# Kernel optimization log

Measured on AMD Instinct MI355X. Metric: run time of the kernel, lower is better.

## Reference

```python
import jax, jax.numpy as jnp
import numpy as np

N_NODES = 50000
N_EDGES = 600000
IN_CH = 128
HID = 128   # 2 * out_channels
OUT = 64


def setup_inputs() -> dict:
    key = jax.random.key(0)
    ks = jax.random.split(key, 8)
    x = jax.random.normal(ks[0], (N_NODES, IN_CH), dtype=jnp.float32)
    edge_index = jax.random.randint(ks[1], (2, N_EDGES), 0, N_NODES, dtype=jnp.int64)
    edge_weight = jax.random.uniform(ks[2], (N_EDGES,), dtype=jnp.float32)
    # GCNConv params: glorot-style linear weight (no lin bias), plus conv bias
    W1 = jax.random.normal(ks[3], (IN_CH, HID), dtype=jnp.float32) / np.sqrt(IN_CH)
    b1 = jnp.zeros((HID,), dtype=jnp.float32)
    W2 = jax.random.normal(ks[4], (HID, OUT), dtype=jnp.float32) / np.sqrt(HID)
    b2 = jnp.zeros((OUT,), dtype=jnp.float32)
    return {"x": x, "edge_index": edge_index, "edge_weight": edge_weight,
            "W1": W1, "b1": b1, "W2": W2, "b2": b2}


def reference(x, edge_index, edge_weight, W1, b1, W2, b2):
    n = x.shape[0]
    row, col = edge_index[0], edge_index[1]
    # gcn_norm with add_self_loops=True (self-loop weight = 1.0):
    # deg[j] = sum_{(i,j) in E} w_ij + 1
    deg = jax.ops.segment_sum(edge_weight, col, num_segments=n) + 1.0
    dis = jnp.where(deg > 0, jax.lax.rsqrt(deg), 0.0)  # deg^{-1/2}
    norm = dis[row] * edge_weight * dis[col]           # [E]
    self_norm = dis * dis                              # [N], self-loop weight 1

    def gcn(h, W, b):
        hW = h @ W                                      # [N, F_out]
        # gather source features, scale by norm, scatter-add to destinations
        agg = jax.ops.segment_sum(norm[:, None] * hW[row], col, num_segments=n)
        return agg + self_norm[:, None] * hW + b

    h = jax.nn.elu(gcn(x, W1, b1))
    alpha = jax.nn.softplus(gcn(h, W2, b2)) + 1e-4
    return alpha
```

## Files before the change

### kernel.cpp

```cpp
#include <hip/hip_runtime.h>
#include <math.h>

typedef unsigned int uint32;
typedef __attribute__((ext_vector_type(8))) short bf16x8;
typedef __attribute__((ext_vector_type(4))) float f32x4;

#define CAP 64

__device__ inline unsigned short f2bf(float f) {
    unsigned int u = __float_as_uint(f);
    return (unsigned short)((u + 0x7fffu + ((u >> 16) & 1u)) >> 16);
}
__device__ inline float bf2f(unsigned short u) {
    return __uint_as_float((unsigned int)u << 16);
}
__device__ inline float softplus_f(float x) {
    return fmaxf(x, 0.f) + log1pf(expf(-fabsf(x)));
}


template<int NC, bool BF16IN>
__device__ void mfma_gemm_body(const void* Xv, const float* __restrict__ W,
                               unsigned short* __restrict__ tabY, int M, int bid) {
    constexpr int PAD = 40;
    __shared__ unsigned short As[128 * PAD];
    __shared__ unsigned short Bs[NC * PAD];

    const int t = threadIdx.x;
    const int lane = t & 63;
    const int wv = t >> 6;
    const int row0 = bid * 128;
    const int l15 = lane & 15, l4 = lane >> 4;

    const int wrow = (NC == 128) ? (wv >> 1) * 64 : wv * 32;
    const int wcol = (NC == 128) ? (wv & 1) * 64 : 0;
    constexpr int NI = (NC == 128) ? 4 : 2;
    constexpr int NJ = 4;

    f32x4 acc[NI][NJ];
#pragma unroll
    for (int i = 0; i < NI; ++i)
#pragma unroll
        for (int j = 0; j < NJ; ++j) acc[i][j] = (f32x4)(0.f);

    for (int k0 = 0; k0 < 128; k0 += 32) {
        __syncthreads();
        if (BF16IN) {
            const unsigned short* X = (const unsigned short*)Xv;
#pragma unroll
            for (int q = 0; q < 2; ++q) {
                int chunk = t * 2 + q;
                int r = chunk >> 2, k8 = chunk & 3;
                int gr = row0 + r;
                uint4 v = make_uint4(0, 0, 0, 0);
                if (gr < M) v = *(const uint4*)&X[(size_t)gr * 128 + k0 + k8 * 8];
                *(uint4*)&As[r * PAD + k8 * 8] = v;
            }
        } else {
            const float* X = (const float*)Xv;
#pragma unroll
            for (int q = 0; q < 4; ++q) {
                int chunk = t * 4 + q;
                int r = chunk >> 3, k4 = chunk & 7;
                int gr = row0 + r;
                float4 v = make_float4(0.f, 0.f, 0.f, 0.f);
                if (gr < M) v = *(const float4*)&X[(size_t)gr * 128 + k0 + k4 * 4];
                ushort4 o;
                o.x = f2bf(v.x); o.y = f2bf(v.y); o.z = f2bf(v.z); o.w = f2bf(v.w);
                *(ushort4*)&As[r * PAD + k4 * 4] = o;
            }
        }
        if (NC == 128) {
#pragma unroll
            for (int q = 0; q < 4; ++q) {
                int chunk = t * 4 + q;
                int kr = chunk >> 5, c4 = chunk & 31;
                float4 v = *(const float4*)&W[(size_t)(k0 + kr) * NC + c4 * 4];
                Bs[(c4 * 4 + 0) * PAD + kr] = f2bf(v.x);
                Bs[(c4 * 4 + 1) * PAD + kr] = f2bf(v.y);
                Bs[(c4 * 4 + 2) * PAD + kr] = f2bf(v.z);
                Bs[(c4 * 4 + 3) * PAD + kr] = f2bf(v.w);
            }
        } else {
#pragma unroll
            for (int q = 0; q < 2; ++q) {
                int chunk = t * 2 + q;
                int kr = chunk >> 4, c4 = chunk & 15;
                float4 v = *(const float4*)&W[(size_t)(k0 + kr) * NC + c4 * 4];
                Bs[(c4 * 4 + 0) * PAD + kr] = f2bf(v.x);
                Bs[(c4 * 4 + 1) * PAD + kr] = f2bf(v.y);
                Bs[(c4 * 4 + 2) * PAD + kr] = f2bf(v.z);
                Bs[(c4 * 4 + 3) * PAD + kr] = f2bf(v.w);
            }
        }
        __syncthreads();

        bf16x8 af[NI], bfr[NJ];
#pragma unroll
        for (int i = 0; i < NI; ++i)
            af[i] = *(const bf16x8*)&As[(wrow + i * 16 + l15) * PAD + l4 * 8];
#pragma unroll
        for (int j = 0; j < NJ; ++j)
            bfr[j] = *(const bf16x8*)&Bs[(wcol + j * 16 + l15) * PAD + l4 * 8];
#pragma unroll
        for (int i = 0; i < NI; ++i)
#pragma unroll
            for (int j = 0; j < NJ; ++j)
                acc[i][j] = __builtin_amdgcn_mfma_f32_16x16x32_bf16(
                    af[i], bfr[j], acc[i][j], 0, 0, 0);
    }

#pragma unroll
    for (int i = 0; i < NI; ++i)
#pragma unroll
        for (int r = 0; r < 4; ++r) {
            int grow = row0 + wrow + i * 16 + l4 * 4 + r;
            if (grow < M) {
#pragma unroll
                for (int j = 0; j < NJ; ++j)
                    tabY[(size_t)grow * NC + wcol + j * 16 + l15] = f2bf(acc[i][j][r]);
            }
        }
}


__global__ __launch_bounds__(256) void k_fused1(const float* __restrict__ X,
                                                const float* __restrict__ W,
                                                unsigned short* __restrict__ tabY, int M,
                                                const int* __restrict__ row,
                                                const int* __restrict__ col,
                                                const float* __restrict__ ew,
                                                int* __restrict__ cnt,
                                                uint32* __restrict__ csr,
                                                int E, int Ggemm) {
    if ((int)blockIdx.x < Ggemm) {
        mfma_gemm_body<128, false>(X, W, tabY, M, blockIdx.x);
    } else {
        int e = (blockIdx.x - Ggemm) * 256 + threadIdx.x;
        if (e < E) {
            int c = col[e];
            int pos = atomicAdd(&cnt[c], 1);
            if (pos < CAP)
                csr[(size_t)c * CAP + pos] = ((uint32)f2bf(ew[e]) << 16) | (uint32)row[e];
        }
    }
}

__global__ __launch_bounds__(256) void k_gemm64(const unsigned short* __restrict__ H,
                                                const float* __restrict__ W,
                                                unsigned short* __restrict__ tabY, int M) {
    mfma_gemm_body<64, true>(H, W, tabY, M, blockIdx.x);
}

__global__ void k_deg_dis(uint32* __restrict__ csr, const int* __restrict__ cnt,
                          float* __restrict__ dis, int n) {
    int i = blockIdx.x * 256 + threadIdx.x;
    if (i >= n) return;
    int deg = min(cnt[i], CAP);
    size_t beg = (size_t)i * CAP;
    float s = 1.0f;
    for (int p = 0; p < deg; ++p) s += bf2f(csr[beg + p] >> 16);
    dis[i] = rsqrtf(s);
    int pe = (deg + 3) & ~3;
    for (int p = deg; p < pe; ++p) csr[beg + p] = 0;
}


__global__ __launch_bounds__(256) void k_agg128(const unsigned short* __restrict__ tab,
                                                const uint32* __restrict__ csr,
                                                const int* __restrict__ cnt,
                                                const float* __restrict__ dis,
                                                const float* __restrict__ b,
                                                unsigned short* __restrict__ hout, int N) {
    int node = blockIdx.x * 4 + (threadIdx.x >> 6);
    if (node >= N) return;
    int lane = threadIdx.x & 63;
    int li = lane & 31, grp = lane >> 5;
    int deg = min(cnt[node], CAP);
    size_t beg = (size_t)node * CAP;

    float a0 = 0.f, a1 = 0.f, a2 = 0.f, a3 = 0.f;

    for (int p = 0; p < deg; p += 4) {
        uint4 c4 = *(const uint4*)&csr[beg + p];
        uint32 ea = grp ? c4.y : c4.x;
        uint32 eb = grp ? c4.w : c4.z;
        int sa = ea & 0xffffu;
        int sb = eb & 0xffffu;
        float wa = bf2f((unsigned short)(ea >> 16)) * dis[sa];
        float wb = bf2f((unsigned short)(eb >> 16)) * dis[sb];
        ushort4 ta = *(const ushort4*)&tab[(size_t)sa * 128 + li * 4];
        ushort4 tb = *(const ushort4*)&tab[(size_t)sb * 128 + li * 4];
        a0 = fmaf(wa, bf2f(ta.x), a0); a1 = fmaf(wa, bf2f(ta.y), a1);
        a2 = fmaf(wa, bf2f(ta.z), a2); a3 = fmaf(wa, bf2f(ta.w), a3);
        a0 = fmaf(wb, bf2f(tb.x), a0); a1 = fmaf(wb, bf2f(tb.y), a1);
        a2 = fmaf(wb, bf2f(tb.z), a2); a3 = fmaf(wb, bf2f(tb.w), a3);
    }
    a0 += __shfl_xor(a0, 32);
    a1 += __shfl_xor(a1, 32);
    a2 += __shfl_xor(a2, 32);
    a3 += __shfl_xor(a3, 32);

    if (grp == 0) {
        float d = dis[node], sn = d * d;
        ushort4 hv = *(const ushort4*)&tab[(size_t)node * 128 + li * 4];
        float4 bb = *(const float4*)&b[li * 4];
        float v0 = d * a0 + sn * bf2f(hv.x) + bb.x;
        float v1 = d * a1 + sn * bf2f(hv.y) + bb.y;
        float v2 = d * a2 + sn * bf2f(hv.z) + bb.z;
        float v3 = d * a3 + sn * bf2f(hv.w) + bb.w;
        v0 = v0 > 0.f ? v0 : expm1f(v0);
        v1 = v1 > 0.f ? v1 : expm1f(v1);
        v2 = v2 > 0.f ? v2 : expm1f(v2);
        v3 = v3 > 0.f ? v3 : expm1f(v3);
        ushort4 o;
        o.x = f2bf(v0); o.y = f2bf(v1); o.z = f2bf(v2); o.w = f2bf(v3);
        *(ushort4*)&hout[(size_t)node * 128 + li * 4] = o;
    }
}

__global__ __launch_bounds__(256) void k_agg64(const unsigned short* __restrict__ tab,
                                               const uint32* __restrict__ csr,
                                               const int* __restrict__ cnt,
                                               const float* __restrict__ dis,
                                               const float* __restrict__ b,
                                               float* __restrict__ out, int N) {
    int node = blockIdx.x * 4 + (threadIdx.x >> 6);
    if (node >= N) return;
    int lane = threadIdx.x & 63;
    int li = lane & 31, grp = lane >> 5;
    int deg = min(cnt[node], CAP);
    size_t beg = (size_t)node * CAP;

    float a0 = 0.f, a1 = 0.f;

    for (int p = 0; p < deg; p += 4) {
        uint4 c4 = *(const uint4*)&csr[beg + p];
        uint32 ea = grp ? c4.y : c4.x;
        uint32 eb = grp ? c4.w : c4.z;
        int sa = ea & 0xffffu;
        int sb = eb & 0xffffu;
        float wa = bf2f((unsigned short)(ea >> 16)) * dis[sa];
        float wb = bf2f((unsigned short)(eb >> 16)) * dis[sb];
        ushort2 ta = *(const ushort2*)&tab[(size_t)sa * 64 + li * 2];
        ushort2 tb = *(const ushort2*)&tab[(size_t)sb * 64 + li * 2];
        a0 = fmaf(wa, bf2f(ta.x), a0); a1 = fmaf(wa, bf2f(ta.y), a1);
        a0 = fmaf(wb, bf2f(tb.x), a0); a1 = fmaf(wb, bf2f(tb.y), a1);
    }
    a0 += __shfl_xor(a0, 32);
    a1 += __shfl_xor(a1, 32);

    if (grp == 0) {
        float d = dis[node], sn = d * d;
        ushort2 hv = *(const ushort2*)&tab[(size_t)node * 64 + li * 2];
        float2 bb = *(const float2*)&b[li * 2];
        float v0 = d * a0 + sn * bf2f(hv.x) + bb.x;
        float v1 = d * a1 + sn * bf2f(hv.y) + bb.y;
        v0 = softplus_f(v0) + 1e-4f;
        v1 = softplus_f(v1) + 1e-4f;
        *(float2*)&out[(size_t)node * 64 + li * 2] = make_float2(v0, v1);
    }
}


extern "C" void kernel_launch(void* const* d_in, const int* in_sizes, int n_in,
                              void* d_out, int out_size, void* d_ws, size_t ws_size,
                              hipStream_t stream) {
    const float* x  = (const float*)d_in[0];
    const int*   ei = (const int*)d_in[1];
    const float* ew = (const float*)d_in[2];
    const float* W1 = (const float*)d_in[3];
    const float* b1 = (const float*)d_in[4];
    const float* W2 = (const float*)d_in[5];
    const float* b2 = (const float*)d_in[6];

    const int N = in_sizes[0] / 128;
    const int E = in_sizes[2];
    const int* row = ei;
    const int* col = ei + E;

    const int Na = (N + 63) & ~63;

    char* base = (char*)d_ws;
    float*  dis  = (float*)base;                    base += (size_t)Na * 4;
    int*    cnt  = (int*)base;                      base += (size_t)Na * 4;
    uint32* csr  = (uint32*)base;                   base += (size_t)Na * CAP * 4;
    unsigned short* tab1 = (unsigned short*)base;   base += (size_t)N * 128 * 2;
    unsigned short* h    = (unsigned short*)base;   base += (size_t)N * 128 * 2;
    unsigned short* tab2 = (unsigned short*)base;   base += (size_t)N * 64 * 2;

    const int gN = (N + 255) / 256;
    const int gE = (E + 255) / 256;
    const int Ggemm = (N + 127) / 128;

    hipMemsetAsync(cnt, 0, (size_t)N * 4, stream);

    k_fused1<<<Ggemm + gE, 256, 0, stream>>>(x, W1, tab1, N, row, col, ew,
                                             cnt, csr, E, Ggemm);

    k_deg_dis<<<gN, 256, 0, stream>>>(csr, cnt, dis, N);

    k_agg128<<<(N + 3) / 4, 256, 0, stream>>>(tab1, csr, cnt, dis, b1, h, N);

    k_gemm64<<<Ggemm, 256, 0, stream>>>(h, W2, tab2, N);
    k_agg64<<<(N + 3) / 4, 256, 0, stream>>>(tab2, csr, cnt, dis, b2,
                                             (float*)d_out, N);
}
```

Before: 126.8 us.

## Prescale features by deg^-1/2 to drop per-edge dis gathers in aggregation

Factors the symmetric normalization so source rows are prescaled by dis (a new warp-per-node kernel for layer 1, the GEMM epilogue for layer 2). The aggregation loops then no longer gather dis[src] per edge. The degree computation becomes a wave-wide shuffle reduction, the epilogues use both half-waves with fast exp/log intrinsics, and the loop runs to the padded degree. The cost is an extra read-modify-write of tab1 and slightly different bf16 rounding and transcendental accuracy.

```diff
diff --git a/kernel.cpp b/kernel.cpp
--- a/kernel.cpp
+++ b/kernel.cpp
@@ -14,13 +14,17 @@
 __device__ inline float bf2f(unsigned short u) {
     return __uint_as_float((unsigned int)u << 16);
 }
-__device__ inline float softplus_f(float x) {
-    return fmaxf(x, 0.f) + log1pf(expf(-fabsf(x)));
-}
-
-
-template<int NC, bool BF16IN>
+__device__ inline float softplus_fast(float x) {
+    return fmaxf(x, 0.f) + __logf(1.f + __expf(-fabsf(x)));
+}
+__device__ inline float elu_fast(float v) {
+    return v > 0.f ? v : (__expf(v) - 1.f);
+}
+
+
+template<int NC, bool BF16IN, bool SCALE>
 __device__ void mfma_gemm_body(const void* Xv, const float* __restrict__ W,
+                               const float* __restrict__ dscale,
                                unsigned short* __restrict__ tabY, int M, int bid) {
     constexpr int PAD = 40;
     __shared__ unsigned short As[128 * PAD];
@@ -116,9 +120,11 @@
         for (int r = 0; r < 4; ++r) {
             int grow = row0 + wrow + i * 16 + l4 * 4 + r;
             if (grow < M) {
+                float dd = SCALE ? dscale[grow] : 1.0f;
 #pragma unroll
                 for (int j = 0; j < NJ; ++j)
-                    tabY[(size_t)grow * NC + wcol + j * 16 + l15] = f2bf(acc[i][j][r]);
+                    tabY[(size_t)grow * NC + wcol + j * 16 + l15] =
+                        f2bf(dd * acc[i][j][r]);
             }
         }
 }
@@ -134,7 +140,7 @@
                                                 uint32* __restrict__ csr,
                                                 int E, int Ggemm) {
     if ((int)blockIdx.x < Ggemm) {
-        mfma_gemm_body<128, false>(X, W, tabY, M, blockIdx.x);
+        mfma_gemm_body<128, false, false>(X, W, nullptr, tabY, M, blockIdx.x);
     } else {
         int e = (blockIdx.x - Ggemm) * 256 + threadIdx.x;
         if (e < E) {
@@ -148,21 +154,35 @@
 
 __global__ __launch_bounds__(256) void k_gemm64(const unsigned short* __restrict__ H,
                                                 const float* __restrict__ W,
+                                                const float* __restrict__ dis,
                                                 unsigned short* __restrict__ tabY, int M) {
-    mfma_gemm_body<64, true>(H, W, tabY, M, blockIdx.x);
-}
-
-__global__ void k_deg_dis(uint32* __restrict__ csr, const int* __restrict__ cnt,
-                          float* __restrict__ dis, int n) {
-    int i = blockIdx.x * 256 + threadIdx.x;
-    if (i >= n) return;
-    int deg = min(cnt[i], CAP);
-    size_t beg = (size_t)i * CAP;
-    float s = 1.0f;
-    for (int p = 0; p < deg; ++p) s += bf2f(csr[beg + p] >> 16);
-    dis[i] = rsqrtf(s);
-    int pe = (deg + 3) & ~3;
-    for (int p = deg; p < pe; ++p) csr[beg + p] = 0;
+    mfma_gemm_body<64, true, true>(H, W, dis, tabY, M, blockIdx.x);
+}
+
+
+__global__ __launch_bounds__(256) void k_disscale(uint32* __restrict__ csr,
+                                                  const int* __restrict__ cnt,
+                                                  float* __restrict__ dis,
+                                                  unsigned short* __restrict__ tab1,
+                                                  int N) {
+    int node = blockIdx.x * 4 + (threadIdx.x >> 6);
+    if (node >= N) return;
+    int lane = threadIdx.x & 63;
+    int deg = min(cnt[node], CAP);
+    int degp = (deg + 3) & ~3;
+    size_t beg = (size_t)node * CAP;
+
+    float w = (lane < deg) ? bf2f((unsigned short)(csr[beg + lane] >> 16)) : 0.f;
+    if (lane >= deg && lane < degp) csr[beg + lane] = 0;
+#pragma unroll
+    for (int m = 1; m < 64; m <<= 1) w += __shfl_xor(w, m);
+    float d = rsqrtf(1.f + w);
+    if (lane == 0) dis[node] = d;
+
+    ushort2 t = *(const ushort2*)&tab1[(size_t)node * 128 + lane * 2];
+    t.x = f2bf(d * bf2f(t.x));
+    t.y = f2bf(d * bf2f(t.y));
+    *(ushort2*)&tab1[(size_t)node * 128 + lane * 2] = t;
 }
 
 
@@ -177,18 +197,17 @@
     int lane = threadIdx.x & 63;
     int li = lane & 31, grp = lane >> 5;
     int deg = min(cnt[node], CAP);
+    int degp = (deg + 3) & ~3;
     size_t beg = (size_t)node * CAP;
 
     float a0 = 0.f, a1 = 0.f, a2 = 0.f, a3 = 0.f;
 
-    for (int p = 0; p < deg; p += 4) {
+    for (int p = 0; p < degp; p += 4) {
         uint4 c4 = *(const uint4*)&csr[beg + p];
         uint32 ea = grp ? c4.y : c4.x;
         uint32 eb = grp ? c4.w : c4.z;
-        int sa = ea & 0xffffu;
-        int sb = eb & 0xffffu;
-        float wa = bf2f((unsigned short)(ea >> 16)) * dis[sa];
-        float wb = bf2f((unsigned short)(eb >> 16)) * dis[sb];
+        int sa = ea & 0xffffu; float wa = bf2f((unsigned short)(ea >> 16));
+        int sb = eb & 0xffffu; float wb = bf2f((unsigned short)(eb >> 16));
         ushort4 ta = *(const ushort4*)&tab[(size_t)sa * 128 + li * 4];
         ushort4 tb = *(const ushort4*)&tab[(size_t)sb * 128 + li * 4];
         a0 = fmaf(wa, bf2f(ta.x), a0); a1 = fmaf(wa, bf2f(ta.y), a1);
@@ -201,22 +220,17 @@
     a2 += __shfl_xor(a2, 32);
     a3 += __shfl_xor(a3, 32);
 
-    if (grp == 0) {
-        float d = dis[node], sn = d * d;
-        ushort4 hv = *(const ushort4*)&tab[(size_t)node * 128 + li * 4];
-        float4 bb = *(const float4*)&b[li * 4];
-        float v0 = d * a0 + sn * bf2f(hv.x) + bb.x;
-        float v1 = d * a1 + sn * bf2f(hv.y) + bb.y;
-        float v2 = d * a2 + sn * bf2f(hv.z) + bb.z;
-        float v3 = d * a3 + sn * bf2f(hv.w) + bb.w;
-        v0 = v0 > 0.f ? v0 : expm1f(v0);
-        v1 = v1 > 0.f ? v1 : expm1f(v1);
-        v2 = v2 > 0.f ? v2 : expm1f(v2);
-        v3 = v3 > 0.f ? v3 : expm1f(v3);
-        ushort4 o;
-        o.x = f2bf(v0); o.y = f2bf(v1); o.z = f2bf(v2); o.w = f2bf(v3);
-        *(ushort4*)&hout[(size_t)node * 128 + li * 4] = o;
-    }
+    int c0 = li * 4 + grp * 2;
+    float s0 = grp ? a2 : a0;
+    float s1 = grp ? a3 : a1;
+    float d = dis[node];
+    ushort2 hv = *(const ushort2*)&tab[(size_t)node * 128 + c0];
+    float2 bb = *(const float2*)&b[c0];
+    float v0 = elu_fast(d * (s0 + bf2f(hv.x)) + bb.x);
+    float v1 = elu_fast(d * (s1 + bf2f(hv.y)) + bb.y);
+    ushort2 o;
+    o.x = f2bf(v0); o.y = f2bf(v1);
+    *(ushort2*)&hout[(size_t)node * 128 + c0] = o;
 }
 
 __global__ __launch_bounds__(256) void k_agg64(const unsigned short* __restrict__ tab,
@@ -230,18 +244,17 @@
     int lane = threadIdx.x & 63;
     int li = lane & 31, grp = lane >> 5;
     int deg = min(cnt[node], CAP);
+    int degp = (deg + 3) & ~3;
     size_t beg = (size_t)node * CAP;
 
     float a0 = 0.f, a1 = 0.f;
 
-    for (int p = 0; p < deg; p += 4) {
+    for (int p = 0; p < degp; p += 4) {
         uint4 c4 = *(const uint4*)&csr[beg + p];
         uint32 ea = grp ? c4.y : c4.x;
         uint32 eb = grp ? c4.w : c4.z;
-        int sa = ea & 0xffffu;
-        int sb = eb & 0xffffu;
-        float wa = bf2f((unsigned short)(ea >> 16)) * dis[sa];
-        float wb = bf2f((unsigned short)(eb >> 16)) * dis[sb];
+        int sa = ea & 0xffffu; float wa = bf2f((unsigned short)(ea >> 16));
+        int sb = eb & 0xffffu; float wb = bf2f((unsigned short)(eb >> 16));
         ushort2 ta = *(const ushort2*)&tab[(size_t)sa * 64 + li * 2];
         ushort2 tb = *(const ushort2*)&tab[(size_t)sb * 64 + li * 2];
         a0 = fmaf(wa, bf2f(ta.x), a0); a1 = fmaf(wa, bf2f(ta.y), a1);
@@ -250,16 +263,12 @@
     a0 += __shfl_xor(a0, 32);
     a1 += __shfl_xor(a1, 32);
 
-    if (grp == 0) {
-        float d = dis[node], sn = d * d;
-        ushort2 hv = *(const ushort2*)&tab[(size_t)node * 64 + li * 2];
-        float2 bb = *(const float2*)&b[li * 2];
-        float v0 = d * a0 + sn * bf2f(hv.x) + bb.x;
-        float v1 = d * a1 + sn * bf2f(hv.y) + bb.y;
-        v0 = softplus_f(v0) + 1e-4f;
-        v1 = softplus_f(v1) + 1e-4f;
-        *(float2*)&out[(size_t)node * 64 + li * 2] = make_float2(v0, v1);
-    }
+    int c = li * 2 + grp;
+    float s = grp ? a1 : a0;
+    float d = dis[node];
+    float hv = bf2f(tab[(size_t)node * 64 + c]);
+    float v = d * (s + hv) + b[c];
+    out[(size_t)node * 64 + c] = softplus_fast(v) + 1e-4f;
 }
 
 
@@ -289,20 +298,19 @@
     unsigned short* h    = (unsigned short*)base;   base += (size_t)N * 128 * 2;
     unsigned short* tab2 = (unsigned short*)base;   base += (size_t)N * 64 * 2;
 
-    const int gN = (N + 255) / 256;
     const int gE = (E + 255) / 256;
     const int Ggemm = (N + 127) / 128;
+    const int gW = (N + 3) / 4;
 
     hipMemsetAsync(cnt, 0, (size_t)N * 4, stream);
 
     k_fused1<<<Ggemm + gE, 256, 0, stream>>>(x, W1, tab1, N, row, col, ew,
                                              cnt, csr, E, Ggemm);
 
-    k_deg_dis<<<gN, 256, 0, stream>>>(csr, cnt, dis, N);
-
-    k_agg128<<<(N + 3) / 4, 256, 0, stream>>>(tab1, csr, cnt, dis, b1, h, N);
-
-    k_gemm64<<<Ggemm, 256, 0, stream>>>(h, W2, tab2, N);
-    k_agg64<<<(N + 3) / 4, 256, 0, stream>>>(tab2, csr, cnt, dis, b2,
-                                             (float*)d_out, N);
-}
+    k_disscale<<<gW, 256, 0, stream>>>(csr, cnt, dis, tab1, N);
+
+    k_agg128<<<gW, 256, 0, stream>>>(tab1, csr, cnt, dis, b1, h, N);
+
+    k_gemm64<<<Ggemm, 256, 0, stream>>>(h, W2, dis, tab2, N);
+    k_agg64<<<gW, 256, 0, stream>>>(tab2, csr, cnt, dis, b2, (float*)d_out, N);
+}
```

Result: no change. 125.1 us (-1.3%).
